# Kernel optimization log

Hardware: AMD Instinct MI355X
Metric: run time of the kernel (lower is better)

The kernel has to match this reference:

```python
import jax, jax.numpy as jnp
import numpy as np

BIG_CONST = 1000000.0
LN_EPS = 1e-5

B, S, D = 2, 1024, 1024
N, H = 16, D // 16            # n_head, d_head
POS_LEN = 2 * S - 1


def setup_inputs() -> dict:
    key = jax.random.key(0)
    ks = jax.random.split(key, 16)
    std_qkv = np.sqrt(1.0 / float(D + N * H))   # EinsumLayer init: 1/sqrt(fan_in+fan_out)
    std_post = np.sqrt(1.0 / float(N * H + D))
    return {
        "q": jax.random.normal(ks[0], (B, S, D), jnp.float32),
        "k": jax.random.normal(ks[1], (B, S, D), jnp.float32),
        "v": jax.random.normal(ks[2], (B, S, D), jnp.float32),
        "pos_enc": jax.random.normal(ks[3], (POS_LEN, D), jnp.float32),
        "attn_mask": jax.random.randint(ks[4], (B, 1, 1, S), 0, 2, jnp.int32),
        "q_w": jax.random.normal(ks[5], (D, N, H), jnp.float32) * std_qkv,
        "k_w": jax.random.normal(ks[6], (D, N, H), jnp.float32) * std_qkv,
        "k_b": jnp.zeros((N, H), jnp.float32),
        "v_w": jax.random.normal(ks[7], (D, N, H), jnp.float32) * std_qkv,
        "v_b": jnp.zeros((N, H), jnp.float32),
        "r_w_bias": jax.random.uniform(ks[8], (N, 1, H), jnp.float32, 0.0, 0.1),
        "r_r_bias": jax.random.uniform(ks[9], (N, 1, H), jnp.float32, 0.0, 0.1),
        "r_kernel": jax.random.uniform(ks[10], (N, D, H), jnp.float32, 0.0, 0.1),
        "post_w": jax.random.normal(ks[11], (N, H, D), jnp.float32) * std_post,
        "post_b": jnp.zeros((D,), jnp.float32),
        "ln_g": jnp.ones((D,), jnp.float32),
        "ln_b": jnp.zeros((D,), jnp.float32),
    }


def reference(q, k, v, pos_enc, attn_mask, q_w, k_w, k_b, v_w, v_b,
              r_w_bias, r_r_bias, r_kernel, post_w, post_b, ln_g, ln_b):
    input_q = q
    d_head = q_w.shape[-1]
    normalizer = 1.0 / np.sqrt(d_head)

    # head projections -> [B, N, L, H]
    qh = jnp.einsum('bld,dnh->bnlh', q, q_w)
    kh = jnp.einsum('bld,dnh->bnlh', k, k_w) + k_b[None, :, None, :] * 0 + jnp.transpose(k_b, (0, 1))[None, :, None, :] * 0 + k_b.reshape(1, k_b.shape[0], 1, k_b.shape[1])
    kh = jnp.einsum('bld,dnh->bnlh', k, k_w) + k_b.reshape(1, -1, 1, d_head)
    vh = jnp.einsum('bld,dnh->bnlh', v, v_w) + v_b.reshape(1, -1, 1, d_head)

    # content score: (q + r_w_bias) @ k^T * normalizer   [B,N,S,S]
    content = jnp.einsum('bnqh,bnkh->bnqk', qh + r_w_bias[None], kh) * normalizer

    # positional term (rel_shift with shift=0): r = pos_enc @ r_kernel -> [N, P, H]
    r = jnp.einsum('pd,ndh->nph', pos_enc, r_kernel)
    pos_scores = jnp.einsum('bnqh,nph->bnqp', qh + r_r_bias[None], r) * normalizer
    # shift=0 => reshape-swap + narrow + reshape-back is an exact identity; then narrow to k_len
    k_len = kh.shape[-2]
    pos_term = pos_scores[..., :k_len]

    attn_score = (content + pos_term).astype(jnp.float32)
    attn_score = attn_score - BIG_CONST * attn_mask.astype(jnp.float32)
    attn_dist = jax.nn.softmax(attn_score, axis=-1)

    out = jnp.einsum('bnqk,bnkh->bnqh', attn_dist, vh)          # [B,N,S,H]
    attn_out = jnp.einsum('bnlh,nhd->bld', out, post_w) + post_b

    x = input_q + attn_out
    mu = jnp.mean(x, axis=-1, keepdims=True)
    var = jnp.mean(jnp.square(x - mu), axis=-1, keepdims=True)
    return (x - mu) / jnp.sqrt(var + LN_EPS) * ln_g + ln_b
```

## Files before the change

kernel.cpp:

```cpp
#include <hip/hip_runtime.h>
#include <cstddef>
#include <cstdint>

typedef unsigned short u16;
typedef unsigned int   u32;

#define S_LEN  1024
#define NHEAD  16
#define HDIM   64
#define DMODEL 1024
#define NORMSC 0.125f
#define BIGC   1000000.0f
#define LOG2E  1.44269504088896f
#define SC2    (0.125f * 1.44269504088896f)

typedef __bf16 bf16x8 __attribute__((ext_vector_type(8)));
typedef float  f32x4  __attribute__((ext_vector_type(4)));

#define MFMA16(a, b, c) __builtin_amdgcn_mfma_f32_16x16x32_bf16((a), (b), (c), 0, 0, 0)

__device__ __forceinline__ u16 f2bf(float f) {
    u32 u = __float_as_uint(f);
    u32 r = (u + 0x7fffu + ((u >> 16) & 1u)) >> 16;
    return (u16)r;
}
__device__ __forceinline__ float bf2f(u32 v) {
    return __uint_as_float(v << 16);
}
__device__ __forceinline__ float4 unp4(uint2 u) {
    float4 f;
    f.x = bf2f(u.x & 0xffffu); f.y = bf2f(u.x >> 16);
    f.z = bf2f(u.y & 0xffffu); f.w = bf2f(u.y >> 16);
    return f;
}
__device__ __forceinline__ void async16(const void* g, void* l) {
    __builtin_amdgcn_global_load_lds(
        (__attribute__((address_space(1))) void*)(g),
        (__attribute__((address_space(3))) void*)(l), 16, 0, 0);
}

__global__ __launch_bounds__(256) void prep_all(
    const float* q, const float* k, const float* v, const float* pos,
    const float* qw, const float* kw, const float* vw, const float* pw, const float* rk,
    u16* qbf, u16* kbf, u16* vbf, u16* posb,
    u16* qwT, u16* kwT, u16* vwT, u16* pwT, u16* WrT)
{
    __shared__ float tb[32][33];
    const int bid = blockIdx.x, tid = threadIdx.x;
    if (bid < 7168) {
        const float* s; u16* d; int base;
        if (bid < 2048)      { s = q;   d = qbf;  base = bid; }
        else if (bid < 4096) { s = k;   d = kbf;  base = bid - 2048; }
        else if (bid < 6144) { s = v;   d = vbf;  base = bid - 4096; }
        else                 { s = pos; d = posb; base = bid - 6144; }
        const int i = base * 1024 + tid * 4;
        const float4 val = *(const float4*)&s[i];
        uint2 o;
        o.x = (u32)f2bf(val.x) | ((u32)f2bf(val.y) << 16);
        o.y = (u32)f2bf(val.z) | ((u32)f2bf(val.w) << 16);
        *(uint2*)&d[i] = o;
        return;
    }
    const int t = bid - 7168;
    const float* in; u16* out; int ild, r0, c0;
    if (t < 4096) {
        const int ts = t & 1023;
        if (t < 1024)      { in = qw; out = qwT; }
        else if (t < 2048) { in = kw; out = kwT; }
        else if (t < 3072) { in = vw; out = vwT; }
        else               { in = pw; out = pwT; }
        ild = 1024;
        r0 = (ts >> 5) * 32; c0 = (ts & 31) * 32;
    } else {
        const int ts = t - 4096;
        const int n = ts >> 6, tt = ts & 63;
        in = rk + (size_t)n * 65536; out = WrT + (size_t)n * 65536;
        ild = 64;
        r0 = (tt >> 1) * 32; c0 = (tt & 1) * 32;
    }
    const int tx = tid & 31, ty = tid >> 5;
    for (int i = ty; i < 32; i += 8)
        tb[i][tx] = in[(size_t)(r0 + i) * ild + c0 + tx];
    __syncthreads();
    for (int i = ty; i < 32; i += 8)
        out[(size_t)(c0 + i) * 1024 + r0 + tx] = f2bf(tb[tx][i]);
}

struct GJ { const u16* A; const u16* Bt; u16* C; int M; int k0; int klen; };

__global__ __launch_bounds__(256) void gemm_p(
    GJ j0, GJ j1, GJ j2, GJ j3, GJ j4, GJ j5, GJ j6, GJ j7)
{
    GJ g;
    switch (blockIdx.z) {
        case 0: g = j0; break; case 1: g = j1; break;
        case 2: g = j2; break; case 3: g = j3; break;
        case 4: g = j4; break; case 5: g = j5; break;
        case 6: g = j6; break; default: g = j7;
    }
    const int bm = blockIdx.y * 128;
    if (bm >= g.M) return;
    const int bn = blockIdx.x * 128;
    __shared__ u16 As[4096];
    __shared__ u16 Bs[4096];
    const int tid = threadIdx.x;
    const int w = tid >> 6, lane = tid & 63;
    const int wm = (w >> 1) * 64, wn = (w & 1) * 64;
    const int l15 = lane & 15, l16 = lane >> 4;
    f32x4 acc[4][4] = {};
    const char* Ab = (const char*)g.A;
    const char* Bb = (const char*)g.Bt;
    const int kend = g.k0 + g.klen;
    for (int k0 = g.k0; k0 < kend; k0 += 32) {
        __syncthreads();
#pragma unroll
        for (int i = 0; i < 2; ++i) {
            const int m = (i * 4 + w) * 1024 + lane * 16;
            const int r = m >> 6, cb = m & 63;
            async16(Ab + ((size_t)(bm + r) * 1024 + k0) * 2 + cb, (char*)As + m);
            async16(Bb + ((size_t)(bn + r) * 1024 + k0) * 2 + cb, (char*)Bs + m);
        }
        __syncthreads();
        bf16x8 af[4], bfr[4];
#pragma unroll
        for (int i = 0; i < 4; ++i)
            af[i] = *(const bf16x8*)&As[(wm + i * 16 + l15) * 32 + l16 * 8];
#pragma unroll
        for (int j = 0; j < 4; ++j)
            bfr[j] = *(const bf16x8*)&Bs[(wn + j * 16 + l15) * 32 + l16 * 8];
#pragma unroll
        for (int i = 0; i < 4; ++i)
#pragma unroll
            for (int j = 0; j < 4; ++j)
                acc[i][j] = MFMA16(af[i], bfr[j], acc[i][j]);
    }
#pragma unroll
    for (int i = 0; i < 4; ++i)
#pragma unroll
        for (int j = 0; j < 4; ++j) {
            const int c = bn + wn + j * 16 + l15;
#pragma unroll
            for (int rg = 0; rg < 4; ++rg) {
                const int m = bm + wm + i * 16 + l16 * 4 + rg;
                g.C[(size_t)m * 1024 + c] = f2bf(acc[i][j][rg]);
            }
        }
}

__global__ __launch_bounds__(256) void prep2(
    const u16* pk0, const u16* pk1, const u16* pr0, const u16* pr1,
    const u16* pv0, const u16* pv1, const u16* pq0, const u16* pq1,
    const float* kbi, const float* vbi, const float* rwb, const float* rrb,
    const int* mask, u16* keff, float* cc, u16* vT, u16* qhb)
{
    __shared__ float tb[32][33];
    const int bid = blockIdx.x, tid = threadIdx.x;
    if (bid < 2048) {
        const int t = bid * 256 + tid;
        const int row = t >> 4, li = t & 15;
        const int n = (row >> 10) & 15, kk = row & 1023, b = row >> 14;
        const size_t mi = ((size_t)(b * 1024 + kk)) * 1024 + n * 64 + li * 4;
        const size_t pi = ((size_t)kk) * 1024 + n * 64 + li * 4;
        const float4 k0v = unp4(*(const uint2*)&pk0[mi]);
        const float4 k1v = unp4(*(const uint2*)&pk1[mi]);
        const float4 r0v = unp4(*(const uint2*)&pr0[pi]);
        const float4 r1v = unp4(*(const uint2*)&pr1[pi]);
        const float4 kb4 = *(const float4*)&kbi[n * 64 + li * 4];
        float4 kv, rv;
        kv.x = k0v.x + k1v.x + kb4.x; kv.y = k0v.y + k1v.y + kb4.y;
        kv.z = k0v.z + k1v.z + kb4.z; kv.w = k0v.w + k1v.w + kb4.w;
        rv.x = r0v.x + r1v.x; rv.y = r0v.y + r1v.y;
        rv.z = r0v.z + r1v.z; rv.w = r0v.w + r1v.w;
        const float4 w1 = *(const float4*)&rwb[n * 64 + li * 4];
        const float4 w2 = *(const float4*)&rrb[n * 64 + li * 4];
        float s = w1.x * kv.x + w1.y * kv.y + w1.z * kv.z + w1.w * kv.w
                + w2.x * rv.x + w2.y * rv.y + w2.z * rv.z + w2.w * rv.w;
        uint2 o;
        o.x = (u32)f2bf(kv.x + rv.x) | ((u32)f2bf(kv.y + rv.y) << 16);
        o.y = (u32)f2bf(kv.z + rv.z) | ((u32)f2bf(kv.w + rv.w) << 16);
        *(uint2*)&keff[(size_t)row * 64 + li * 4] = o;
#pragma unroll
        for (int m = 1; m < 16; m <<= 1) s += __shfl_xor(s, m);
        if (li == 0)
            cc[row] = LOG2E * (NORMSC * s - BIGC * (float)mask[b * 1024 + kk]);
        return;
    }
    if (bid < 4096) {
        const int t = bid - 2048;
        const int head = t >> 6, tt = t & 63;
        const int b = head >> 4, n = head & 15;
        const int r0 = (tt >> 1) * 32, c0 = (tt & 1) * 32;
        const int tx = tid & 31, ty = tid >> 5;
        const float vb = vbi[n * 64 + c0 + tx];
        for (int i = ty; i < 32; i += 8) {
            const size_t idx = ((size_t)(b * 1024 + r0 + i)) * 1024 + n * 64 + c0 + tx;
            tb[i][tx] = bf2f(pv0[idx]) + bf2f(pv1[idx]) + vb;
        }
        __syncthreads();
        u16* out = vT + (size_t)head * 65536;
        for (int i = ty; i < 32; i += 8)
            out[(size_t)(c0 + i) * 1024 + r0 + tx] = f2bf(tb[tx][i]);
        return;
    }
    const int t = bid - 4096;
    const int e = t * 1024 + tid * 4;
    const int m = e >> 10, c = e & 1023;
    const float4 a = unp4(*(const uint2*)&pq0[e]);
    const float4 b4 = unp4(*(const uint2*)&pq1[e]);
    uint2 o;
    o.x = (u32)f2bf(a.x + b4.x) | ((u32)f2bf(a.y + b4.y) << 16);
    o.y = (u32)f2bf(a.z + b4.z) | ((u32)f2bf(a.w + b4.w) << 16);
    const int b2 = m >> 10, l = m & 1023, n = c >> 6, h = c & 63;
    *(uint2*)&qhb[(((size_t)(b2 * NHEAD + n)) * 1024 + l) * 64 + h] = o;
}

__global__ __launch_bounds__(256) void attn_mfma(
    const u16* qb, const u16* kb, const u16* vtb, const float* ccomb,
    float* o0, float* o1, float* lsb0, float* lsb1)
{
    __shared__ u16   Ks[8192];
    __shared__ u16   Vs[8192];
    __shared__ __bf16 Ps[4][1024];
    const int tid = threadIdx.x;
    const int w = tid >> 6, lane = tid & 63;
    const int l15 = lane & 15, l16 = lane >> 4;
    const int ks = blockIdx.x >> 9;
    const int r = blockIdx.x & 511;
    const int head = r >> 4;
    const int q0 = (r & 15) * 64;
    const int b = head >> 4, n = head & 15;
    const size_t hoff = (size_t)head * 65536;
    const u16* qh = qb + hoff;
    const char* khc = (const char*)(kb + hoff);
    const char* vtc = (const char*)(vtb + hoff);
    const float* cc = ccomb + head * 1024;
    float* Op = ks ? o1 : o0;
    float* ls = ks ? lsb1 : lsb0;
    __bf16* Pw = Ps[w];

    bf16x8 qf[2];
    {
        const size_t rb = ((size_t)(q0 + w * 16 + l15)) * 64 + l16 * 8;
        qf[0] = *(const bf16x8*)&qh[rb];
        qf[1] = *(const bf16x8*)&qh[rb + 32];
    }
    f32x4 Oacc[4] = {};
    float lsum[4] = {};

    for (int kc = ks * 4; kc < ks * 4 + 4; ++kc) {
        __syncthreads();
#pragma unroll
        for (int i = 0; i < 4; ++i) {
            const int m = (i * 4 + w) * 1024 + lane * 16;
            const int kr = m >> 7, kcc = (m >> 4) & 7;
            async16(khc + kc * 16384 + kr * 128 + (((kcc + kr) & 7) << 4), (char*)Ks + m);
            const int vr = m >> 8, vc = (m >> 4) & 15;
            async16(vtc + (size_t)vr * 2048 + kc * 256 + (((vc + vr) & 15) << 4), (char*)Vs + m);
        }
        __syncthreads();

        f32x4 sc[8];
#pragma unroll
        for (int j = 0; j < 8; ++j) {
            const int rk2 = j * 16 + l15;
            const int base = rk2 * 64;
            f32x4 a = {0.f, 0.f, 0.f, 0.f};
            a = MFMA16(qf[0], *(const bf16x8*)&Ks[base + (((l16 - rk2) & 7) << 3)], a);
            a = MFMA16(qf[1], *(const bf16x8*)&Ks[base + (((l16 + 4 - rk2) & 7) << 3)], a);
            const float cadd = cc[kc * 128 + j * 16 + l15];
            sc[j] = a * SC2 + cadd;
        }
#pragma unroll
        for (int h2 = 0; h2 < 2; ++h2) {
#pragma unroll
            for (int j2 = 0; j2 < 4; ++j2) {
                const int j = h2 * 4 + j2;
                const int cg = j2 * 2 + (l15 >> 3);
#pragma unroll
                for (int rg = 0; rg < 4; ++rg) {
                    const float p = exp2f(sc[j][rg]);
                    lsum[rg] += p;
                    const int row = l16 * 4 + rg;
                    Pw[row * 64 + (((cg - row) & 7) << 3) + (l15 & 7)] = (__bf16)p;
                }
            }
            bf16x8 pf[2];
#pragma unroll
            for (int f = 0; f < 2; ++f)
                pf[f] = *(const bf16x8*)&Pw[l15 * 64 + (((f * 4 + l16 - l15) & 7) << 3)];
#pragma unroll
            for (int t4 = 0; t4 < 4; ++t4) {
#pragma unroll
                for (int f = 0; f < 2; ++f) {
                    const int vr = t4 * 16 + l15;
                    const int ch = h2 * 8 + f * 4 + l16;
                    const bf16x8 vf = *(const bf16x8*)&Vs[vr * 128 + (((ch - vr) & 15) << 3)];
                    Oacc[t4] = MFMA16(pf[f], vf, Oacc[t4]);
                }
            }
        }
    }
#pragma unroll
    for (int t4 = 0; t4 < 4; ++t4)
#pragma unroll
        for (int rg = 0; rg < 4; ++rg) {
            const int srow = q0 + w * 16 + l16 * 4 + rg;
            const int col = n * 64 + t4 * 16 + l15;
            Op[((size_t)b * 1024 + srow) * 1024 + col] = Oacc[t4][rg];
        }
    float4 s4;
#pragma unroll
    for (int rg = 0; rg < 4; ++rg) {
        float s = lsum[rg];
#pragma unroll
        for (int m = 1; m < 16; m <<= 1) s += __shfl_xor(s, m);
        ((float*)&s4)[rg] = s;
    }
    if (l15 == 0)
        *(float4*)&ls[head * 1024 + q0 + w * 16 + l16 * 4] = s4;
}

__global__ __launch_bounds__(256) void comb_o(
    const float* o0, const float* o1, const float* ls0, const float* ls1, u16* Obf)
{
    const int i = (blockIdx.x * 256 + threadIdx.x) * 4;
    const int row = i >> 10, col = i & 1023;
    const int b = row >> 10, s = row & 1023, n = col >> 6;
    const int head = b * 16 + n;
    const float inv = 1.0f / (ls0[head * 1024 + s] + ls1[head * 1024 + s]);
    const float4 a = *(const float4*)&o0[i];
    const float4 c = *(const float4*)&o1[i];
    uint2 o;
    o.x = (u32)f2bf((a.x + c.x) * inv) | ((u32)f2bf((a.y + c.y) * inv) << 16);
    o.y = (u32)f2bf((a.z + c.z) * inv) | ((u32)f2bf((a.w + c.w) * inv) << 16);
    *(uint2*)&Obf[i] = o;
}

__global__ __launch_bounds__(256) void ln_kernel(
    const u16* __restrict__ p0, const u16* __restrict__ p1,
    const u16* __restrict__ p2, const u16* __restrict__ p3,
    const float* __restrict__ resid, const float* __restrict__ pb,
    const float* __restrict__ g, const float* __restrict__ bb,
    float* __restrict__ out)
{
    const int row = blockIdx.x;
    const int tid = threadIdx.x;
    const size_t i = (size_t)row * DMODEL + tid * 4;
    const float4 a0 = unp4(*(const uint2*)&p0[i]);
    const float4 a1 = unp4(*(const uint2*)&p1[i]);
    const float4 a2 = unp4(*(const uint2*)&p2[i]);
    const float4 a3 = unp4(*(const uint2*)&p3[i]);
    const float4 rr = *(const float4*)&resid[i];
    const float4 pv = *(const float4*)&pb[tid * 4];
    float4 v;
    v.x = a0.x + a1.x + a2.x + a3.x + rr.x + pv.x;
    v.y = a0.y + a1.y + a2.y + a3.y + rr.y + pv.y;
    v.z = a0.z + a1.z + a2.z + a3.z + rr.z + pv.z;
    v.w = a0.w + a1.w + a2.w + a3.w + rr.w + pv.w;
    float s1 = v.x + v.y + v.z + v.w;
    float s2 = v.x * v.x + v.y * v.y + v.z * v.z + v.w * v.w;
#pragma unroll
    for (int off = 32; off; off >>= 1) {
        s1 += __shfl_down(s1, off);
        s2 += __shfl_down(s2, off);
    }
    __shared__ float rb[8];
    if ((tid & 63) == 0) { rb[tid >> 6] = s1; rb[4 + (tid >> 6)] = s2; }
    __syncthreads();
    if (tid == 0) {
        rb[0] = rb[0] + rb[1] + rb[2] + rb[3];
        rb[4] = rb[4] + rb[5] + rb[6] + rb[7];
    }
    __syncthreads();
    s1 = rb[0]; s2 = rb[4];
    const float mu = s1 * (1.0f / DMODEL);
    const float var = s2 * (1.0f / DMODEL) - mu * mu;
    const float rstd = rsqrtf(var + 1e-5f);
    const float4 gv = *(const float4*)&g[tid * 4];
    const float4 bv = *(const float4*)&bb[tid * 4];
    float4 o;
    o.x = (v.x - mu) * rstd * gv.x + bv.x;
    o.y = (v.y - mu) * rstd * gv.y + bv.y;
    o.z = (v.z - mu) * rstd * gv.z + bv.z;
    o.w = (v.w - mu) * rstd * gv.w + bv.w;
    *(float4*)&out[i] = o;
}

extern "C" void kernel_launch(void* const* d_in, const int* in_sizes, int n_in,
                              void* d_out, int out_size, void* d_ws, size_t ws_size,
                              hipStream_t stream)
{
    (void)in_sizes; (void)n_in; (void)out_size; (void)ws_size;
    const float* q   = (const float*)d_in[0];
    const float* k   = (const float*)d_in[1];
    const float* v   = (const float*)d_in[2];
    const float* pos = (const float*)d_in[3];
    const int*   msk = (const int*)d_in[4];
    const float* qw  = (const float*)d_in[5];
    const float* kw  = (const float*)d_in[6];
    const float* kbi = (const float*)d_in[7];
    const float* vw  = (const float*)d_in[8];
    const float* vbi = (const float*)d_in[9];
    const float* rwb = (const float*)d_in[10];
    const float* rrb = (const float*)d_in[11];
    const float* rk  = (const float*)d_in[12];
    const float* pw  = (const float*)d_in[13];
    const float* pb  = (const float*)d_in[14];
    const float* lg  = (const float*)d_in[15];
    const float* lb  = (const float*)d_in[16];
    float* out = (float*)d_out;

    float* fb = (float*)d_ws;
    float* cc   = fb;
    float* ls0  = cc + 32768;
    float* ls1  = ls0 + 32768;
    float* Op0  = ls1 + 32768;
    float* Op1  = Op0 + 2097152;
    u16* us   = (u16*)(Op1 + 2097152);
    u16* qbf  = us;
    u16* kbf  = qbf + 2097152;
    u16* vbf  = kbf + 2097152;
    u16* posb = vbf + 2097152;
    u16* qwT  = posb + 1048576;
    u16* kwT  = qwT + 1048576;
    u16* vwT  = kwT + 1048576;
    u16* pwT  = vwT + 1048576;
    u16* WrT  = pwT + 1048576;
    u16* qhb  = WrT + 1048576;
    u16* keffb= qhb + 2097152;
    u16* vTb  = keffb + 2097152;
    u16* pq0  = vTb + 2097152;
    u16* pq1  = pq0 + 2097152;
    u16* pk0  = pq1 + 2097152;
    u16* pk1  = pk0 + 2097152;
    u16* pv0  = pk1 + 2097152;
    u16* pv1  = pv0 + 2097152;
    u16* pr0  = pv1 + 2097152;
    u16* pr1  = pr0 + 1048576;
    u16* po0  = pr1 + 1048576;
    u16* po1  = po0 + 2097152;
    u16* po2  = po1 + 2097152;
    u16* po3  = po2 + 2097152;
    u16* Obf  = qbf;

    dim3 blk(256);
    prep_all<<<12288, blk, 0, stream>>>(q, k, v, pos, qw, kw, vw, pw, rk,
                                        qbf, kbf, vbf, posb, qwT, kwT, vwT, pwT, WrT);

    GJ jq0 = {qbf,  qwT, pq0, 2048, 0,   512};
    GJ jq1 = {qbf,  qwT, pq1, 2048, 512, 512};
    GJ jk0 = {kbf,  kwT, pk0, 2048, 0,   512};
    GJ jk1 = {kbf,  kwT, pk1, 2048, 512, 512};
    GJ jv0 = {vbf,  vwT, pv0, 2048, 0,   512};
    GJ jv1 = {vbf,  vwT, pv1, 2048, 512, 512};
    GJ jp0 = {posb, WrT, pr0, 1024, 0,   512};
    GJ jp1 = {posb, WrT, pr1, 1024, 512, 512};
    gemm_p<<<dim3(8, 16, 8), blk, 0, stream>>>(jq0, jq1, jk0, jk1, jv0, jv1, jp0, jp1);

    prep2<<<6144, blk, 0, stream>>>(pk0, pk1, pr0, pr1, pv0, pv1, pq0, pq1,
                                    kbi, vbi, rwb, rrb, msk, keffb, cc, vTb, qhb);

    attn_mfma<<<1024, blk, 0, stream>>>(qhb, keffb, vTb, cc, Op0, Op1, ls0, ls1);

    comb_o<<<2048, blk, 0, stream>>>(Op0, Op1, ls0, ls1, Obf);

    GJ jo0 = {Obf, pwT, po0, 2048, 0,   256};
    GJ jo1 = {Obf, pwT, po1, 2048, 256, 256};
    GJ jo2 = {Obf, pwT, po2, 2048, 512, 256};
    GJ jo3 = {Obf, pwT, po3, 2048, 768, 256};
    gemm_p<<<dim3(8, 16, 4), blk, 0, stream>>>(jo0, jo1, jo2, jo3, jo0, jo0, jo0, jo0);

    ln_kernel<<<2048, blk, 0, stream>>>(po0, po1, po2, po3, q, pb, lg, lb, out);
}
```

Measured before the change: 226.5 us.

## Drop split-K attention and fuse normalization into attention kernel

The attention kernel no longer splits the key range across two blocks with separate partial outputs. Each 128-thread block now handles 32 query rows over all 1024 keys in 64-key chunks, normalizes in registers and writes bf16 output directly, which removes the comb_o kernel and the fp32 partial-output traffic. The trade-off is smaller blocks with less K/V reuse per staged tile and more loop iterations per block, plus changed shared-memory swizzles.

Result: no change. 224.5 us (-0.9%).

```diff
diff --git a/kernel.cpp b/kernel.cpp
--- a/kernel.cpp
+++ b/kernel.cpp
@@ -214,28 +214,23 @@
     *(uint2*)&qhb[(((size_t)(b2 * NHEAD + n)) * 1024 + l) * 64 + h] = o;
 }
 
-__global__ __launch_bounds__(256) void attn_mfma(
-    const u16* qb, const u16* kb, const u16* vtb, const float* ccomb,
-    float* o0, float* o1, float* lsb0, float* lsb1)
-{
-    __shared__ u16   Ks[8192];
-    __shared__ u16   Vs[8192];
-    __shared__ __bf16 Ps[4][1024];
+__global__ __launch_bounds__(128) void attn_mfma(
+    const u16* qb, const u16* kb, const u16* vtb, const float* ccomb, u16* O)
+{
+    __shared__ u16   Ks[4096];
+    __shared__ u16   Vs[4096];
+    __shared__ __bf16 Ps[2][1024];
     const int tid = threadIdx.x;
     const int w = tid >> 6, lane = tid & 63;
     const int l15 = lane & 15, l16 = lane >> 4;
-    const int ks = blockIdx.x >> 9;
-    const int r = blockIdx.x & 511;
-    const int head = r >> 4;
-    const int q0 = (r & 15) * 64;
+    const int head = blockIdx.x >> 5;
+    const int q0 = (blockIdx.x & 31) * 32;
     const int b = head >> 4, n = head & 15;
     const size_t hoff = (size_t)head * 65536;
     const u16* qh = qb + hoff;
     const char* khc = (const char*)(kb + hoff);
     const char* vtc = (const char*)(vtb + hoff);
     const float* cc = ccomb + head * 1024;
-    float* Op = ks ? o1 : o0;
-    float* ls = ks ? lsb1 : lsb0;
     __bf16* Pw = Ps[w];
 
     bf16x8 qf[2];
@@ -247,93 +242,73 @@
     f32x4 Oacc[4] = {};
     float lsum[4] = {};
 
-    for (int kc = ks * 4; kc < ks * 4 + 4; ++kc) {
+    for (int kc = 0; kc < 16; ++kc) {
         __syncthreads();
 #pragma unroll
         for (int i = 0; i < 4; ++i) {
-            const int m = (i * 4 + w) * 1024 + lane * 16;
-            const int kr = m >> 7, kcc = (m >> 4) & 7;
-            async16(khc + kc * 16384 + kr * 128 + (((kcc + kr) & 7) << 4), (char*)Ks + m);
-            const int vr = m >> 8, vc = (m >> 4) & 15;
-            async16(vtc + (size_t)vr * 2048 + kc * 256 + (((vc + vr) & 15) << 4), (char*)Vs + m);
+            const int r = w * 32 + i * 8 + (lane >> 3);
+            const int c = lane & 7;
+            async16(khc + kc * 8192 + r * 128 + (((c + r) & 7) << 4),
+                    (char*)Ks + r * 128 + c * 16);
+            async16(vtc + (size_t)r * 2048 + kc * 128 + (((c + r) & 7) << 4),
+                    (char*)Vs + r * 128 + c * 16);
         }
         __syncthreads();
 
-        f32x4 sc[8];
-#pragma unroll
-        for (int j = 0; j < 8; ++j) {
+        f32x4 sc[4];
+#pragma unroll
+        for (int j = 0; j < 4; ++j) {
             const int rk2 = j * 16 + l15;
             const int base = rk2 * 64;
             f32x4 a = {0.f, 0.f, 0.f, 0.f};
             a = MFMA16(qf[0], *(const bf16x8*)&Ks[base + (((l16 - rk2) & 7) << 3)], a);
             a = MFMA16(qf[1], *(const bf16x8*)&Ks[base + (((l16 + 4 - rk2) & 7) << 3)], a);
-            const float cadd = cc[kc * 128 + j * 16 + l15];
+            const float cadd = cc[kc * 64 + j * 16 + l15];
             sc[j] = a * SC2 + cadd;
         }
 #pragma unroll
-        for (int h2 = 0; h2 < 2; ++h2) {
-#pragma unroll
-            for (int j2 = 0; j2 < 4; ++j2) {
-                const int j = h2 * 4 + j2;
-                const int cg = j2 * 2 + (l15 >> 3);
-#pragma unroll
-                for (int rg = 0; rg < 4; ++rg) {
-                    const float p = exp2f(sc[j][rg]);
-                    lsum[rg] += p;
-                    const int row = l16 * 4 + rg;
-                    Pw[row * 64 + (((cg - row) & 7) << 3) + (l15 & 7)] = (__bf16)p;
-                }
+        for (int j = 0; j < 4; ++j) {
+            const int cg = j * 2 + (l15 >> 3);
+#pragma unroll
+            for (int rg = 0; rg < 4; ++rg) {
+                const float p = exp2f(sc[j][rg]);
+                lsum[rg] += p;
+                const int row = l16 * 4 + rg;
+                Pw[row * 64 + (((cg - row) & 7) << 3) + (l15 & 7)] = (__bf16)p;
             }
-            bf16x8 pf[2];
-#pragma unroll
-            for (int f = 0; f < 2; ++f)
-                pf[f] = *(const bf16x8*)&Pw[l15 * 64 + (((f * 4 + l16 - l15) & 7) << 3)];
-#pragma unroll
-            for (int t4 = 0; t4 < 4; ++t4) {
-#pragma unroll
-                for (int f = 0; f < 2; ++f) {
-                    const int vr = t4 * 16 + l15;
-                    const int ch = h2 * 8 + f * 4 + l16;
-                    const bf16x8 vf = *(const bf16x8*)&Vs[vr * 128 + (((ch - vr) & 15) << 3)];
-                    Oacc[t4] = MFMA16(pf[f], vf, Oacc[t4]);
-                }
+        }
+        bf16x8 pf[2];
+#pragma unroll
+        for (int f = 0; f < 2; ++f)
+            pf[f] = *(const bf16x8*)&Pw[l15 * 64 + (((f * 4 + l16 - l15) & 7) << 3)];
+#pragma unroll
+        for (int t4 = 0; t4 < 4; ++t4) {
+#pragma unroll
+            for (int f = 0; f < 2; ++f) {
+                const int vr = t4 * 16 + l15;
+                const int ch = f * 4 + l16;
+                const bf16x8 vf = *(const bf16x8*)&Vs[vr * 64 + (((ch - vr) & 7) << 3)];
+                Oacc[t4] = MFMA16(pf[f], vf, Oacc[t4]);
             }
         }
     }
-#pragma unroll
-    for (int t4 = 0; t4 < 4; ++t4)
+    float inv[4];
+#pragma unroll
+    for (int rg = 0; rg < 4; ++rg) {
+        float s = lsum[rg];
+#pragma unroll
+        for (int m = 1; m < 16; m <<= 1) s += __shfl_xor(s, m);
+        inv[rg] = 1.0f / s;
+    }
+#pragma unroll
+    for (int t4 = 0; t4 < 4; ++t4) {
 #pragma unroll
         for (int rg = 0; rg < 4; ++rg) {
             const int srow = q0 + w * 16 + l16 * 4 + rg;
             const int col = n * 64 + t4 * 16 + l15;
-            Op[((size_t)b * 1024 + srow) * 1024 + col] = Oacc[t4][rg];
-        }
-    float4 s4;
-#pragma unroll
-    for (int rg = 0; rg < 4; ++rg) {
-        float s = lsum[rg];
-#pragma unroll
-        for (int m = 1; m < 16; m <<= 1) s += __shfl_xor(s, m);
-        ((float*)&s4)[rg] = s;
-    }
-    if (l15 == 0)
-        *(float4*)&ls[head * 1024 + q0 + w * 16 + l16 * 4] = s4;
-}
-
-__global__ __launch_bounds__(256) void comb_o(
-    const float* o0, const float* o1, const float* ls0, const float* ls1, u16* Obf)
-{
-    const int i = (blockIdx.x * 256 + threadIdx.x) * 4;
-    const int row = i >> 10, col = i & 1023;
-    const int b = row >> 10, s = row & 1023, n = col >> 6;
-    const int head = b * 16 + n;
-    const float inv = 1.0f / (ls0[head * 1024 + s] + ls1[head * 1024 + s]);
-    const float4 a = *(const float4*)&o0[i];
-    const float4 c = *(const float4*)&o1[i];
-    uint2 o;
-    o.x = (u32)f2bf((a.x + c.x) * inv) | ((u32)f2bf((a.y + c.y) * inv) << 16);
-    o.y = (u32)f2bf((a.z + c.z) * inv) | ((u32)f2bf((a.w + c.w) * inv) << 16);
-    *(uint2*)&Obf[i] = o;
+            O[((size_t)b * 1024 + srow) * 1024 + col] = f2bf(Oacc[t4][rg] * inv[rg]);
+        }
+    }
 }
 
 __global__ __launch_bounds__(256) void ln_kernel(
@@ -412,11 +387,7 @@
 
     float* fb = (float*)d_ws;
     float* cc   = fb;
-    float* ls0  = cc + 32768;
-    float* ls1  = ls0 + 32768;
-    float* Op0  = ls1 + 32768;
-    float* Op1  = Op0 + 2097152;
-    u16* us   = (u16*)(Op1 + 2097152);
+    u16* us   = (u16*)(cc + 32768);
     u16* qbf  = us;
     u16* kbf  = qbf + 2097152;
     u16* vbf  = kbf + 2097152;
@@ -460,9 +431,7 @@
     prep2<<<6144, blk, 0, stream>>>(pk0, pk1, pr0, pr1, pv0, pv1, pq0, pq1,
                                     kbi, vbi, rwb, rrb, msk, keffb, cc, vTb, qhb);
 
-    attn_mfma<<<1024, blk, 0, stream>>>(qhb, keffb, vTb, cc, Op0, Op1, ls0, ls1);
-
-    comb_o<<<2048, blk, 0, stream>>>(Op0, Op1, ls0, ls1, Obf);
+    attn_mfma<<<1024, dim3(128), 0, stream>>>(qhb, keffb, vTb, cc, Obf);
 
     GJ jo0 = {Obf, pwT, po0, 2048, 0,   256};
     GJ jo1 = {Obf, pwT, po1, 2048, 256, 256};
```
